# Kernel tuning notes

Hardware: AMD Instinct MI355X
Metric: run time of the kernel (lower is better)

The kernel has to match this reference:

```python
import jax, jax.numpy as jnp
import numpy as np

B, L, D, H = 2, 1024, 1024, 16
HD = D // H  # head_dim = 64


def setup_inputs() -> dict:
    key = jax.random.key(0)
    ks = jax.random.split(key, 6)
    s = 1.0 / np.sqrt(D)
    return {
        "x": jax.random.normal(ks[0], (B, L, D), jnp.float32),
        "structure_bias": jax.random.normal(ks[1], (B, L, D), jnp.float32),
        # weights stored as [in, out] (transposed vs torch nn.Linear)
        "Wqkv": jax.random.normal(ks[2], (D, 3 * D), jnp.float32) * s,
        "bqkv": jnp.zeros((3 * D,), jnp.float32),
        "Ws": jax.random.normal(ks[3], (D, D), jnp.float32) * s,
        "bs": jnp.zeros((D,), jnp.float32),
        "Wo": jax.random.normal(ks[4], (D, D), jnp.float32) * s,
        "bo": jnp.zeros((D,), jnp.float32),
    }


def reference(x, structure_bias, Wqkv, bqkv, Ws, bs, Wo, bo):
    b, l, d = x.shape
    # qkv: [B, L, 3, H, HD] -> (3, B, H, L, HD)
    qkv = (x @ Wqkv + bqkv).reshape(b, l, 3, H, HD).transpose(2, 0, 3, 1, 4)
    q, k, v = qkv[0], qkv[1], qkv[2]
    scale = 1.0 / jnp.sqrt(jnp.float32(HD))
    attn = jnp.einsum("bhld,bhmd->bhlm", q, k) * scale  # [B,H,L,L]
    # structure bias: Linear then view(B, 1, L, L); requires L == feature_dim
    sw = (structure_bias @ Ws + bs).reshape(b, 1, l, l)
    attn = jax.nn.softmax(attn + sw, axis=-1)
    out = jnp.einsum("bhlm,bhmd->bhld", attn, v)  # [B,H,L,HD]
    out = out.transpose(0, 2, 1, 3).reshape(b, l, d)
    return out @ Wo + bo
```

## Files before the change

### kernel.cpp

```cpp
#include <hip/hip_runtime.h>
#include <stdint.h>
#include <stddef.h>


typedef float f32x4 __attribute__((ext_vector_type(4)));
typedef short s16x8 __attribute__((ext_vector_type(8)));
typedef unsigned short u16x8 __attribute__((ext_vector_type(8)));
typedef unsigned short u16x4 __attribute__((ext_vector_type(4)));

__device__ inline unsigned short f2bf(float f) {
    unsigned u = __builtin_bit_cast(unsigned, f);
    u += 0x7fffu + ((u >> 16) & 1u);
    return (unsigned short)(u >> 16);
}

__device__ inline f32x4 mfma16(s16x8 a, s16x8 b, f32x4 c) {
    return __builtin_amdgcn_mfma_f32_16x16x32_bf16(a, b, c, 0, 0, 0);
}

__device__ inline void gld_lds16(const void* g, const void* lds_base) {
    __builtin_amdgcn_global_load_lds(
        (const __attribute__((address_space(1))) void*)(uintptr_t)g,
        (__attribute__((address_space(3))) void*)(unsigned)(uintptr_t)lds_base,
        16, 0, 0);
}

__global__ __launch_bounds__(256) void prep_k(const float* __restrict__ x,
                                              const float* __restrict__ sb,
                                              const float* __restrict__ Wqkv,
                                              const float* __restrict__ Ws,
                                              const float* __restrict__ Wo,
                                              unsigned short* __restrict__ xb,
                                              unsigned short* __restrict__ sbb,
                                              unsigned short* __restrict__ wqkvt,
                                              unsigned short* __restrict__ wst,
                                              unsigned short* __restrict__ wot) {
    __shared__ float tile[64][65];
    const int blk = blockIdx.x, t = threadIdx.x;
    if (blk < 2048) {
        const float* src = (blk < 1024) ? x : sb;
        unsigned short* dst = (blk < 1024) ? xb : sbb;
        int i = (blk & 1023) * 256 + t;
        const float4* s4 = (const float4*)src;
        float4 a = s4[2 * i], b = s4[2 * i + 1];
        u16x8 o;
        o[0] = f2bf(a.x); o[1] = f2bf(a.y); o[2] = f2bf(a.z); o[3] = f2bf(a.w);
        o[4] = f2bf(b.x); o[5] = f2bf(b.y); o[6] = f2bf(b.z); o[7] = f2bf(b.w);
        *(u16x8*)(dst + (size_t)i * 8) = o;
        return;
    }
    int tt = blk - 2048;
    const float* W; unsigned short* Wt; int N, n0, k0;
    if (tt < 768)       { W = Wqkv; Wt = wqkvt; N = 3072; n0 = (tt % 48) * 64; k0 = (tt / 48) * 64; }
    else if (tt < 1024) { tt -= 768;  W = Ws; Wt = wst; N = 1024; n0 = (tt & 15) * 64; k0 = (tt >> 4) * 64; }
    else                { tt -= 1024; W = Wo; Wt = wot; N = 1024; n0 = (tt & 15) * 64; k0 = (tt >> 4) * 64; }
    const int lr = t >> 4, lc = (t & 15) * 4;
#pragma unroll
    for (int rr = 0; rr < 4; rr++) {
        int r = lr + rr * 16;
        float4 v = *(const float4*)(W + (size_t)(k0 + r) * N + n0 + lc);
        tile[r][lc] = v.x; tile[r][lc + 1] = v.y; tile[r][lc + 2] = v.z; tile[r][lc + 3] = v.w;
    }
    __syncthreads();
    const int wn = t >> 3, wk = (t & 7) * 8;
#pragma unroll
    for (int rr = 0; rr < 2; rr++) {
        int n = wn + rr * 32;
        u16x8 o;
#pragma unroll
        for (int j = 0; j < 8; j++) o[j] = f2bf(tile[wk + j][n]);
        *(u16x8*)(Wt + (size_t)(n0 + n) * 1024 + k0 + wk) = o;
    }
}

template <int EPI>
__global__ __launch_bounds__(256, 3) void gemm_k(const unsigned short* __restrict__ A,
                                                 const unsigned short* __restrict__ Bt,
                                                 const float* __restrict__ bias,
                                                 unsigned short* __restrict__ q,
                                                 unsigned short* __restrict__ kk_,
                                                 unsigned short* __restrict__ vt,
                                                 float* __restrict__ outf) {
    __shared__ unsigned short lA[2][4096];
    __shared__ unsigned short lB[2][8192];
    const int t = threadIdx.x;
    const int wave = t >> 6, lane = t & 63, c = lane & 15, g = lane >> 4;
    const int bn0 = blockIdx.x * 128, bm0 = blockIdx.y * 64;
    const int wc = wave * 32;

    size_t aoff[2], boff[4];
#pragma unroll
    for (int j = 0; j < 2; j++) {
        int s = j * 256 + t, row = s >> 3, ch = (s & 7) ^ (row & 7);
        aoff[j] = (size_t)(bm0 + row) * 1024 + ch * 8;
    }
#pragma unroll
    for (int j = 0; j < 4; j++) {
        int s = j * 256 + t, row = s >> 3, ch = (s & 7) ^ (row & 7);
        boff[j] = (size_t)(bn0 + row) * 1024 + ch * 8;
    }
    char* lAb0 = (char*)lA[0]; char* lBb0 = (char*)lB[0];

#define GSTAGE(buf, kt)                                                                  \
    do {                                                                                 \
        _Pragma("unroll")                                                                \
        for (int j = 0; j < 2; j++)                                                      \
            gld_lds16(A + aoff[j] + (kt), lAb0 + (buf) * 8192 + j * 4096 + wave * 1024); \
        _Pragma("unroll")                                                                \
        for (int j = 0; j < 4; j++)                                                      \
            gld_lds16(Bt + boff[j] + (kt), lBb0 + (buf) * 16384 + j * 4096 + wave * 1024);\
    } while (0)

    f32x4 acc[4][2];
#pragma unroll
    for (int i = 0; i < 4; i++)
#pragma unroll
        for (int j = 0; j < 2; j++) acc[i][j] = {0.f, 0.f, 0.f, 0.f};

    GSTAGE(0, 0);
    for (int ks = 0; ks < 16; ++ks) {
        __syncthreads();
        if (ks < 15) GSTAGE((ks + 1) & 1, (ks + 1) * 64);
        const char* aB = lAb0 + (ks & 1) * 8192;
        const char* bB = lBb0 + (ks & 1) * 16384;
#pragma unroll
        for (int kk2 = 0; kk2 < 2; ++kk2) {
            s16x8 af[4], bfr[2];
#pragma unroll
            for (int i = 0; i < 4; i++) {
                int r_ = i * 16 + c;
                af[i] = *(const s16x8*)(aB + r_ * 128 + (((kk2 * 4 + g) ^ (r_ & 7)) << 4));
            }
#pragma unroll
            for (int j = 0; j < 2; j++) {
                int r_ = wc + j * 16 + c;
                bfr[j] = *(const s16x8*)(bB + r_ * 128 + (((kk2 * 4 + g) ^ (r_ & 7)) << 4));
            }
#pragma unroll
            for (int i = 0; i < 4; i++)
#pragma unroll
                for (int j = 0; j < 2; j++)
                    acc[i][j] = mfma16(af[i], bfr[j], acc[i][j]);
        }
    }
#undef GSTAGE

#pragma unroll
    for (int i = 0; i < 4; i++) {
#pragma unroll
        for (int j = 0; j < 2; j++) {
            const int n = bn0 + wc + j * 16 + c;
            const float bv = bias[n];
#pragma unroll
            for (int r = 0; r < 4; r++) {
                const int m = bm0 + i * 16 + g * 4 + r;
                float v = acc[i][j][r] + bv;
                if (EPI == 0) {
                    const int sel = n >> 10, h = (n >> 6) & 15, d = n & 63;
                    const int b_ = m >> 10, l_ = m & 1023;
                    const size_t bh = (size_t)((b_ << 4) + h);
                    unsigned short hv = f2bf(v);
                    if (sel == 0)      q[(bh * 1024 + l_) * 64 + d] = hv;
                    else if (sel == 1) kk_[(bh * 1024 + l_) * 64 + d] = hv;
                    else               vt[(bh * 64 + d) * 1024 + l_] = hv;
                } else {
                    outf[(size_t)m * 1024 + n] = v;
                }
            }
        }
    }
}

__global__ __launch_bounds__(256, 2) void attn_k(const unsigned short* __restrict__ q,
                                                 const unsigned short* __restrict__ k,
                                                 const unsigned short* __restrict__ vt,
                                                 const float* __restrict__ sw,
                                                 unsigned short* __restrict__ ctx) {
    __shared__ unsigned short kbuf[2][4096];
    __shared__ unsigned short vbuf[2][4096];
    __shared__ unsigned short lP[4][640];
    const int t = threadIdx.x, wave = t >> 6, lane = t & 63, c = lane & 15, g = lane >> 4;
    const int blk = blockIdx.x;
    const int qt = blk & 15, bh = blk >> 4, b_ = bh >> 4, h = bh & 15;
    const int qr = qt * 64 + wave * 16;

    const unsigned short* qbase = q + ((size_t)bh * 1024 + qr) * 64;
    s16x8 qf0 = *(const s16x8*)(qbase + (size_t)c * 64 + g * 8);
    s16x8 qf1 = *(const s16x8*)(qbase + (size_t)c * 64 + 32 + g * 8);

    const unsigned short* kg = k + (size_t)bh * 65536;
    const unsigned short* vg = vt + (size_t)bh * 65536;
    const float* swrow = sw + ((size_t)b_ * 1024 + qr + c) * 1024;

    const int s0 = wave * 128 + lane, s1 = s0 + 64;
    const int r0 = s0 >> 3, ch0 = (s0 & 7) ^ (r0 & 7);
    const int r1 = s1 >> 3, ch1 = (s1 & 7) ^ (r1 & 7);

    const float SC  = 0.125f * 1.4426950408889634f;
    const float L2E = 1.4426950408889634f;

    float mr = -1e30f, lr = 0.0f;
    f32x4 acc[4];
#pragma unroll
    for (int nf = 0; nf < 4; nf++) acc[nf] = {0.f, 0.f, 0.f, 0.f};
    unsigned short* wp = lP[wave];
    const int swz = (c & 7);

#define STAGE(buf, kv0)                                                                     \
    do {                                                                                    \
        gld_lds16(kg + (size_t)((kv0) + r0) * 64 + ch0 * 8, (char*)kbuf[buf] + wave * 2048);            \
        gld_lds16(kg + (size_t)((kv0) + r1) * 64 + ch1 * 8, (char*)kbuf[buf] + wave * 2048 + 1024);     \
        gld_lds16(vg + (size_t)r0 * 1024 + (kv0) + ch0 * 8, (char*)vbuf[buf] + wave * 2048);            \
        gld_lds16(vg + (size_t)r1 * 1024 + (kv0) + ch1 * 8, (char*)vbuf[buf] + wave * 2048 + 1024);     \
    } while (0)

    STAGE(0, 0);
    __syncthreads();

    int cur = 0;
    for (int it = 0; it < 16; ++it) {
        const int kv0 = it * 64;
        if (it < 15) STAGE(cur ^ 1, kv0 + 64);
        float4 sws[4];
#pragma unroll
        for (int j = 0; j < 4; j++) sws[j] = *(const float4*)(swrow + kv0 + j * 16 + 4 * g);

        const char* kB = (const char*)kbuf[cur];
        const char* vB = (const char*)vbuf[cur];
#pragma unroll
        for (int ks2 = 0; ks2 < 2; ++ks2) {
            s16x8 kc0 = *(const s16x8*)(kB + ((ks2 * 32 + c) << 7) + (((0 + g) ^ swz) << 4));
            s16x8 kc1 = *(const s16x8*)(kB + ((ks2 * 32 + c) << 7) + (((4 + g) ^ swz) << 4));
            s16x8 kc2 = *(const s16x8*)(kB + ((ks2 * 32 + 16 + c) << 7) + (((0 + g) ^ swz) << 4));
            s16x8 kc3 = *(const s16x8*)(kB + ((ks2 * 32 + 16 + c) << 7) + (((4 + g) ^ swz) << 4));

            __builtin_amdgcn_s_setprio(1);
            f32x4 ss0 = {0.f, 0.f, 0.f, 0.f}, ss1 = {0.f, 0.f, 0.f, 0.f};
            ss0 = mfma16(kc0, qf0, ss0); ss0 = mfma16(kc1, qf1, ss0);
            ss1 = mfma16(kc2, qf0, ss1); ss1 = mfma16(kc3, qf1, ss1);
            __builtin_amdgcn_s_setprio(0);

            float4 swa = sws[2 * ks2], swb = sws[2 * ks2 + 1];
            float z0[4], z1[4];
#pragma unroll
            for (int r = 0; r < 4; r++) {
                z0[r] = ss0[r] * SC + (&swa.x)[r] * L2E;
                z1[r] = ss1[r] * SC + (&swb.x)[r] * L2E;
            }
            float tm = fmaxf(fmaxf(fmaxf(z0[0], z0[1]), fmaxf(z0[2], z0[3])),
                             fmaxf(fmaxf(z1[0], z1[1]), fmaxf(z1[2], z1[3])));
            tm = fmaxf(tm, __shfl_xor(tm, 16, 64));
            tm = fmaxf(tm, __shfl_xor(tm, 32, 64));

            const bool need = __any((int)(tm > mr + 8.0f));
            float mn = mr, f = 1.0f;
            if (need) { mn = fmaxf(mr, tm); f = __builtin_amdgcn_exp2f(mr - mn); }

            float p0[4], p1[4];
#pragma unroll
            for (int r = 0; r < 4; r++) {
                p0[r] = __builtin_amdgcn_exp2f(z0[r] - mn);
                p1[r] = __builtin_amdgcn_exp2f(z1[r] - mn);
            }
            float rs = (p0[0] + p0[1]) + (p0[2] + p0[3]) + (p1[0] + p1[1]) + (p1[2] + p1[3]);
            rs += __shfl_xor(rs, 16, 64);
            rs += __shfl_xor(rs, 32, 64);

            if (need) {
                mr = mn;
                lr = lr * f + rs;
#pragma unroll
                for (int nf = 0; nf < 4; nf++)
#pragma unroll
                    for (int r = 0; r < 4; r++) acc[nf][r] *= f;
            } else {
                lr += rs;
            }

            u16x4 w0, w1;
#pragma unroll
            for (int r = 0; r < 4; r++) { w0[r] = f2bf(p0[r]); w1[r] = f2bf(p1[r]); }
            *(u16x4*)(wp + c * 40 + 4 * g) = w0;
            *(u16x4*)(wp + c * 40 + 16 + 4 * g) = w1;
            s16x8 ap = *(const s16x8*)((const char*)wp + c * 80 + g * 16);

            __builtin_amdgcn_s_setprio(1);
#pragma unroll
            for (int nf = 0; nf < 4; nf++) {
                s16x8 vf = *(const s16x8*)(vB + ((nf * 16 + c) << 7) + ((((ks2 << 2) + g) ^ swz) << 4));
                acc[nf] = mfma16(vf, ap, acc[nf]);
            }
            __builtin_amdgcn_s_setprio(0);
        }
        __syncthreads();
        cur ^= 1;
    }
#undef STAGE

    float inv = 1.0f / lr;
#pragma unroll
    for (int nf = 0; nf < 4; nf++)
#pragma unroll
        for (int r = 0; r < 4; r++) acc[nf][r] *= inv;

    __syncthreads();
    float* scr = (wave < 2) ? ((float*)kbuf + wave * 1088)
                            : ((float*)vbuf + (wave - 2) * 1088);
#pragma unroll
    for (int nf = 0; nf < 4; nf++)
#pragma unroll
        for (int r = 0; r < 4; r++)
            scr[(nf * 16 + 4 * g + r) * 17 + c] = acc[nf][r];
    __syncthreads();
    u16x8 o0, o1;
#pragma unroll
    for (int j = 0; j < 8; j++) o0[j] = f2bf(scr[(g * 16 + j) * 17 + c]);
#pragma unroll
    for (int j = 0; j < 8; j++) o1[j] = f2bf(scr[(g * 16 + 8 + j) * 17 + c]);
    unsigned short* dst = ctx + ((size_t)(b_ << 10) + qr + c) * 1024 + (h << 6) + g * 16;
    *(u16x8*)dst = o0;
    *(u16x8*)(dst + 8) = o1;
}

extern "C" void kernel_launch(void* const* d_in, const int* in_sizes, int n_in,
                              void* d_out, int out_size, void* d_ws, size_t ws_size,
                              hipStream_t stream) {
    const float* x    = (const float*)d_in[0];
    const float* sb   = (const float*)d_in[1];
    const float* Wqkv = (const float*)d_in[2];
    const float* bqkv = (const float*)d_in[3];
    const float* Ws   = (const float*)d_in[4];
    const float* bs   = (const float*)d_in[5];
    const float* Wo   = (const float*)d_in[6];
    const float* bo   = (const float*)d_in[7];
    float* out = (float*)d_out;

    char* ws = (char*)d_ws;
    unsigned short* xb    = (unsigned short*)(ws);
    unsigned short* sbb   = (unsigned short*)(ws + ((size_t)4 << 20));
    unsigned short* wqkvt = (unsigned short*)(ws + ((size_t)8 << 20));
    unsigned short* wst   = (unsigned short*)(ws + ((size_t)14 << 20));
    unsigned short* wot   = (unsigned short*)(ws + ((size_t)16 << 20));
    unsigned short* qb    = (unsigned short*)(ws + ((size_t)18 << 20));
    unsigned short* kb    = (unsigned short*)(ws + ((size_t)22 << 20));
    unsigned short* vtb   = (unsigned short*)(ws + ((size_t)26 << 20));
    float*          swf   = (float*)        (ws + ((size_t)30 << 20));
    unsigned short* ctxb  = (unsigned short*)(ws + ((size_t)38 << 20));

    prep_k<<<dim3(3328), dim3(256), 0, stream>>>(x, sb, Wqkv, Ws, Wo,
                                                 xb, sbb, wqkvt, wst, wot);
    gemm_k<0><<<dim3(24, 32), dim3(256), 0, stream>>>(xb, wqkvt, bqkv, qb, kb, vtb, (float*)nullptr);
    gemm_k<1><<<dim3(8, 32), dim3(256), 0, stream>>>(sbb, wst, bs,
                                                     (unsigned short*)nullptr, (unsigned short*)nullptr,
                                                     (unsigned short*)nullptr, swf);
    attn_k<<<dim3(512), dim3(256), 0, stream>>>(qb, kb, vtb, swf, ctxb);
    gemm_k<1><<<dim3(8, 32), dim3(256), 0, stream>>>(ctxb, wot, bo,
                                                     (unsigned short*)nullptr, (unsigned short*)nullptr,
                                                     (unsigned short*)nullptr, out);
}
```

Baseline: 92.37 us.

## Merge QKV and structure GEMMs into one launch; triple-buffer attention KV loads

The QKV projection and the structure-bias projection GEMMs are merged into a single launch, with block index choosing the operand set, so one grid of 1024 blocks replaces two launches and fills the device better. The attention kernel moves from double to triple buffering of K/V tiles and uses explicit vmcnt waits with raw barriers, so it keeps two tiles in flight and prefetches the structure-bias row one iteration ahead. The GEMM MFMA block also gets raised wave priority. The cost is more LDS in attention, which may lower occupancy, and hand-written waitcnt logic that depends on the exact number of loads each stage issues.

```diff
diff --git a/kernel.cpp b/kernel.cpp
--- a/kernel.cpp
+++ b/kernel.cpp
@@ -73,19 +73,17 @@
     }
 }
 
-template <int EPI>
-__global__ __launch_bounds__(256, 3) void gemm_k(const unsigned short* __restrict__ A,
-                                                 const unsigned short* __restrict__ Bt,
-                                                 const float* __restrict__ bias,
-                                                 unsigned short* __restrict__ q,
-                                                 unsigned short* __restrict__ kk_,
-                                                 unsigned short* __restrict__ vt,
-                                                 float* __restrict__ outf) {
-    __shared__ unsigned short lA[2][4096];
-    __shared__ unsigned short lB[2][8192];
+__device__ __forceinline__ void gemm_body(const unsigned short* __restrict__ A,
+                                          const unsigned short* __restrict__ Bt,
+                                          const float* __restrict__ bias,
+                                          int bn0, int bm0, int epi,
+                                          unsigned short* __restrict__ q,
+                                          unsigned short* __restrict__ kk_,
+                                          unsigned short* __restrict__ vt,
+                                          float* __restrict__ outf,
+                                          unsigned short* lAs, unsigned short* lBs) {
     const int t = threadIdx.x;
     const int wave = t >> 6, lane = t & 63, c = lane & 15, g = lane >> 4;
-    const int bn0 = blockIdx.x * 128, bm0 = blockIdx.y * 64;
     const int wc = wave * 32;
 
     size_t aoff[2], boff[4];
@@ -99,7 +97,7 @@
         int s = j * 256 + t, row = s >> 3, ch = (s & 7) ^ (row & 7);
         boff[j] = (size_t)(bn0 + row) * 1024 + ch * 8;
     }
-    char* lAb0 = (char*)lA[0]; char* lBb0 = (char*)lB[0];
+    char* lAb0 = (char*)lAs; char* lBb0 = (char*)lBs;
 
 #define GSTAGE(buf, kt)                                                                  \
     do {                                                                                 \
@@ -136,11 +134,13 @@
                 int r_ = wc + j * 16 + c;
                 bfr[j] = *(const s16x8*)(bB + r_ * 128 + (((kk2 * 4 + g) ^ (r_ & 7)) << 4));
             }
+            __builtin_amdgcn_s_setprio(1);
 #pragma unroll
             for (int i = 0; i < 4; i++)
 #pragma unroll
                 for (int j = 0; j < 2; j++)
                     acc[i][j] = mfma16(af[i], bfr[j], acc[i][j]);
+            __builtin_amdgcn_s_setprio(0);
         }
     }
 #undef GSTAGE
@@ -155,7 +155,7 @@
             for (int r = 0; r < 4; r++) {
                 const int m = bm0 + i * 16 + g * 4 + r;
                 float v = acc[i][j][r] + bv;
-                if (EPI == 0) {
+                if (epi == 0) {
                     const int sel = n >> 10, h = (n >> 6) & 15, d = n & 63;
                     const int b_ = m >> 10, l_ = m & 1023;
                     const size_t bh = (size_t)((b_ << 4) + h);
@@ -171,13 +171,45 @@
     }
 }
 
+__global__ __launch_bounds__(256, 3) void gemm01_k(const unsigned short* __restrict__ xb,
+                                                   const unsigned short* __restrict__ wqkvt,
+                                                   const float* __restrict__ bqkv,
+                                                   const unsigned short* __restrict__ sbb,
+                                                   const unsigned short* __restrict__ wst,
+                                                   const float* __restrict__ bs,
+                                                   unsigned short* __restrict__ q,
+                                                   unsigned short* __restrict__ kk_,
+                                                   unsigned short* __restrict__ vt,
+                                                   float* __restrict__ swf) {
+    __shared__ unsigned short lA[2][4096];
+    __shared__ unsigned short lB[2][8192];
+    const int bx = blockIdx.x, bm0 = blockIdx.y * 64;
+    if (bx < 24)
+        gemm_body(xb, wqkvt, bqkv, bx * 128, bm0, 0, q, kk_, vt, (float*)nullptr, lA[0], lB[0]);
+    else
+        gemm_body(sbb, wst, bs, (bx - 24) * 128, bm0, 1,
+                  (unsigned short*)nullptr, (unsigned short*)nullptr, (unsigned short*)nullptr,
+                  swf, lA[0], lB[0]);
+}
+
+__global__ __launch_bounds__(256, 3) void gemmo_k(const unsigned short* __restrict__ ctx,
+                                                  const unsigned short* __restrict__ wot,
+                                                  const float* __restrict__ bo,
+                                                  float* __restrict__ out) {
+    __shared__ unsigned short lA[2][4096];
+    __shared__ unsigned short lB[2][8192];
+    gemm_body(ctx, wot, bo, blockIdx.x * 128, blockIdx.y * 64, 1,
+              (unsigned short*)nullptr, (unsigned short*)nullptr, (unsigned short*)nullptr,
+              out, lA[0], lB[0]);
+}
+
 __global__ __launch_bounds__(256, 2) void attn_k(const unsigned short* __restrict__ q,
                                                  const unsigned short* __restrict__ k,
                                                  const unsigned short* __restrict__ vt,
                                                  const float* __restrict__ sw,
                                                  unsigned short* __restrict__ ctx) {
-    __shared__ unsigned short kbuf[2][4096];
-    __shared__ unsigned short vbuf[2][4096];
+    __shared__ unsigned short kbuf[3][4096];
+    __shared__ unsigned short vbuf[3][4096];
     __shared__ unsigned short lP[4][640];
     const int t = threadIdx.x, wave = t >> 6, lane = t & 63, c = lane & 15, g = lane >> 4;
     const int blk = blockIdx.x;
@@ -215,18 +247,25 @@
     } while (0)
 
     STAGE(0, 0);
-    __syncthreads();
-
-    int cur = 0;
+    float4 swc[4];
+#pragma unroll
+    for (int j = 0; j < 4; j++) swc[j] = *(const float4*)(swrow + j * 16 + 4 * g);
+    STAGE(1, 64);
+
     for (int it = 0; it < 16; ++it) {
         const int kv0 = it * 64;
-        if (it < 15) STAGE(cur ^ 1, kv0 + 64);
-        float4 sws[4];
-#pragma unroll
-        for (int j = 0; j < 4; j++) sws[j] = *(const float4*)(swrow + kv0 + j * 16 + 4 * g);
-
-        const char* kB = (const char*)kbuf[cur];
-        const char* vB = (const char*)vbuf[cur];
+        if (it == 15) asm volatile("s_waitcnt vmcnt(0)" ::: "memory");
+        else          asm volatile("s_waitcnt vmcnt(4)" ::: "memory");
+        __builtin_amdgcn_s_barrier();
+        asm volatile("" ::: "memory");
+        const int kvn = (it < 15) ? kv0 + 64 : kv0;
+        float4 swn[4];
+#pragma unroll
+        for (int j = 0; j < 4; j++) swn[j] = *(const float4*)(swrow + kvn + j * 16 + 4 * g);
+        if (it < 14) STAGE((it + 2) % 3, kv0 + 128);
+
+        const char* kB = (const char*)kbuf[it % 3];
+        const char* vB = (const char*)vbuf[it % 3];
 #pragma unroll
         for (int ks2 = 0; ks2 < 2; ++ks2) {
             s16x8 kc0 = *(const s16x8*)(kB + ((ks2 * 32 + c) << 7) + (((0 + g) ^ swz) << 4));
@@ -240,7 +279,7 @@
             ss1 = mfma16(kc2, qf0, ss1); ss1 = mfma16(kc3, qf1, ss1);
             __builtin_amdgcn_s_setprio(0);
 
-            float4 swa = sws[2 * ks2], swb = sws[2 * ks2 + 1];
+            float4 swa = swc[2 * ks2], swb = swc[2 * ks2 + 1];
             float z0[4], z1[4];
 #pragma unroll
             for (int r = 0; r < 4; r++) {
@@ -292,8 +331,8 @@
             }
             __builtin_amdgcn_s_setprio(0);
         }
-        __syncthreads();
-        cur ^= 1;
+#pragma unroll
+        for (int j = 0; j < 4; j++) swc[j] = swn[j];
     }
 #undef STAGE
 
@@ -304,8 +343,7 @@
         for (int r = 0; r < 4; r++) acc[nf][r] *= inv;
 
     __syncthreads();
-    float* scr = (wave < 2) ? ((float*)kbuf + wave * 1088)
-                            : ((float*)vbuf + (wave - 2) * 1088);
+    float* scr = (float*)kbuf + wave * 1088;
 #pragma unroll
     for (int nf = 0; nf < 4; nf++)
 #pragma unroll
@@ -349,12 +387,8 @@
 
     prep_k<<<dim3(3328), dim3(256), 0, stream>>>(x, sb, Wqkv, Ws, Wo,
                                                  xb, sbb, wqkvt, wst, wot);
-    gemm_k<0><<<dim3(24, 32), dim3(256), 0, stream>>>(xb, wqkvt, bqkv, qb, kb, vtb, (float*)nullptr);
-    gemm_k<1><<<dim3(8, 32), dim3(256), 0, stream>>>(sbb, wst, bs,
-                                                     (unsigned short*)nullptr, (unsigned short*)nullptr,
-                                                     (unsigned short*)nullptr, swf);
+    gemm01_k<<<dim3(32, 32), dim3(256), 0, stream>>>(xb, wqkvt, bqkv, sbb, wst, bs,
+                                                     qb, kb, vtb, swf);
     attn_k<<<dim3(512), dim3(256), 0, stream>>>(qb, kb, vtb, swf, ctxb);
-    gemm_k<1><<<dim3(8, 32), dim3(256), 0, stream>>>(ctxb, wot, bo,
-                                                     (unsigned short*)nullptr, (unsigned short*)nullptr,
-                                                     (unsigned short*)nullptr, out);
-}
+    gemmo_k<<<dim3(8, 32), dim3(256), 0, stream>>>(ctxb, wot, bo, out);
+}
```

Result: slower. 95.08 us (+2.9%).
